# Kernel tuning notes

Measured on AMD Instinct MI355X. Metric: run time of the kernel, lower is better.

Reference implementation:

```python
import jax, jax.numpy as jnp
import numpy as np

D_MODEL = 2048
N_HEADS = 16
HEAD_DIM = D_MODEL // N_HEADS
SCALE = HEAD_DIM ** -0.5
LN_EPS = 1e-5
N_LAYERS = 24


def _layernorm(x, g, b):
    mu = jnp.mean(x, axis=-1, keepdims=True)
    var = jnp.mean(jnp.square(x - mu), axis=-1, keepdims=True)
    return (x - mu) * jax.lax.rsqrt(var + LN_EPS) * g + b


def _split_heads(x):  # [B,S,D] -> [B,H,S,hd]
    B, S, _ = x.shape
    return x.reshape(B, S, N_HEADS, HEAD_DIM).transpose(0, 2, 1, 3)


def setup_inputs() -> dict:
    key = jax.random.key(0)
    ks = jax.random.split(key, 12)
    B, St, Si = 2, 2048, 1024
    std_qkv = D_MODEL ** -0.5
    std_o = (2 * N_LAYERS) ** -0.5
    return {
        "q_text": jax.random.normal(ks[0], (B, St, D_MODEL), jnp.float32),
        "q_image": jax.random.normal(ks[1], (B, Si, D_MODEL), jnp.float32),
        "k_text": jax.random.normal(ks[2], (B, St, D_MODEL), jnp.float32),
        "k_image": jax.random.normal(ks[3], (B, Si, D_MODEL), jnp.float32),
        "Wq": jax.random.normal(ks[4], (D_MODEL, D_MODEL), jnp.float32) * std_qkv,
        "Wk": jax.random.normal(ks[5], (D_MODEL, D_MODEL), jnp.float32) * std_qkv,
        "Wv": jax.random.normal(ks[6], (D_MODEL, D_MODEL), jnp.float32) * std_qkv,
        "Wo": jax.random.normal(ks[7], (D_MODEL, D_MODEL), jnp.float32) * std_o,
        "ln_text_g": jnp.ones((D_MODEL,), jnp.float32),
        "ln_text_b": jnp.zeros((D_MODEL,), jnp.float32),
        "ln_image_g": jnp.ones((D_MODEL,), jnp.float32),
        "ln_image_b": jnp.zeros((D_MODEL,), jnp.float32),
    }


def reference(q_text, q_image, k_text, k_image, Wq, Wk, Wv, Wo,
              ln_text_g, ln_text_b, ln_image_g, ln_image_b):
    # Normalize each key modality once, project to K/V, concat along seq.
    kt = _layernorm(k_text, ln_text_g, ln_text_b)
    ki = _layernorm(k_image, ln_image_g, ln_image_b)
    concat_k = jnp.concatenate([_split_heads(kt @ Wk.T), _split_heads(ki @ Wk.T)], axis=2)
    concat_v = jnp.concatenate([_split_heads(kt @ Wv.T), _split_heads(ki @ Wv.T)], axis=2)

    def attend(q, g, b):
        B, S, _ = q.shape
        qn = _layernorm(q, g, b)
        qh = _split_heads(qn @ Wq.T) * SCALE            # [B,H,Sq,hd]
        scores = jnp.einsum('bhqd,bhkd->bhqk', qh, concat_k)
        attn = jax.nn.softmax(scores.astype(jnp.float32), axis=-1).astype(q.dtype)
        out = jnp.einsum('bhqk,bhkd->bhqd', attn, concat_v)
        out = out.transpose(0, 2, 1, 3).reshape(B, S, D_MODEL)
        return out @ Wo.T

    out_text = attend(q_text, ln_text_g, ln_text_b)
    out_image = attend(q_image, ln_image_g, ln_image_b)
    return (out_text, out_image)
```

## Files before the change

kernel.cpp:

```cpp
#include <hip/hip_runtime.h>

typedef __attribute__((ext_vector_type(8))) short bf16x8;
typedef __attribute__((ext_vector_type(4))) float f32x4;
typedef __attribute__((ext_vector_type(8))) unsigned short u16x8;
typedef __attribute__((ext_vector_type(4))) unsigned short u16x4;

#define D_MODEL 2048
#define NH 16
#define HD 128
#define SKV 3072
#define QK_SCALE 0.08838834764831845f

__device__ __forceinline__ unsigned short f2bf(float f) {
  unsigned int u = __float_as_uint(f);
  u += 0x7fffu + ((u >> 16) & 1u);
  return (unsigned short)(u >> 16);
}

typedef __attribute__((address_space(1))) void as1_void;
typedef __attribute__((address_space(3))) void as3_void;
__device__ __forceinline__ void gload_lds16(const void* g, void* l) {
  __builtin_amdgcn_global_load_lds((as1_void*)g, (as3_void*)l, 16, 0, 0);
}

#define MFMA16(a, b, c) __builtin_amdgcn_mfma_f32_16x16x32_bf16((a), (b), (c), 0, 0, 0)

__global__ __launch_bounds__(256) void cvt_w_kernel(
    const float* __restrict__ s0, const float* __restrict__ s1,
    const float* __restrict__ s2, const float* __restrict__ s3,
    unsigned short* __restrict__ dstbase) {
  const int y = blockIdx.y;
  const float* src = (y == 0) ? s0 : (y == 1) ? s1 : (y == 2) ? s2 : s3;
  const float scale = (y == 0) ? QK_SCALE : 1.0f;
  unsigned short* dst = dstbase + (size_t)y * 4194304;
  int i = blockIdx.x * 256 + threadIdx.x;
  const float4* s = (const float4*)src + (size_t)i * 2;
  float4 a = s[0], b = s[1];
  u16x8 r;
  r[0] = f2bf(a.x * scale); r[1] = f2bf(a.y * scale);
  r[2] = f2bf(a.z * scale); r[3] = f2bf(a.w * scale);
  r[4] = f2bf(b.x * scale); r[5] = f2bf(b.y * scale);
  r[6] = f2bf(b.z * scale); r[7] = f2bf(b.w * scale);
  *((u16x8*)dst + i) = r;
}

__global__ __launch_bounds__(256) void ln_kernel(
    const float* __restrict__ x, const float* __restrict__ gw,
    const float* __restrict__ bw, unsigned short* __restrict__ out,
    int spb, int orpb, int obase) {
  const int row = blockIdx.x;
  const int t = threadIdx.x;
  const int b = row / spb, s = row - b * spb;
  const float* xr = x + (size_t)row * D_MODEL;
  unsigned short* orow = out + ((size_t)b * orpb + obase + s) * D_MODEL;

  float4 v0 = *(const float4*)(xr + t * 8);
  float4 v1 = *(const float4*)(xr + t * 8 + 4);
  float sum = v0.x + v0.y + v0.z + v0.w + v1.x + v1.y + v1.z + v1.w;
  float sq  = v0.x*v0.x + v0.y*v0.y + v0.z*v0.z + v0.w*v0.w
            + v1.x*v1.x + v1.y*v1.y + v1.z*v1.z + v1.w*v1.w;
#pragma unroll
  for (int o = 32; o > 0; o >>= 1) {
    sum += __shfl_down(sum, o);
    sq  += __shfl_down(sq, o);
  }
  __shared__ float red[8];
  const int wv = t >> 6, l = t & 63;
  if (l == 0) { red[wv] = sum; red[4 + wv] = sq; }
  __syncthreads();
  sum = red[0] + red[1] + red[2] + red[3];
  sq  = red[4] + red[5] + red[6] + red[7];
  const float mu = sum * (1.0f / 2048.0f);
  const float var = sq * (1.0f / 2048.0f) - mu * mu;
  const float rs = rsqrtf(var + 1e-5f);

  float4 g0 = *(const float4*)(gw + t * 8);
  float4 g1 = *(const float4*)(gw + t * 8 + 4);
  float4 b0 = *(const float4*)(bw + t * 8);
  float4 b1 = *(const float4*)(bw + t * 8 + 4);
  u16x8 r;
  r[0] = f2bf((v0.x - mu) * rs * g0.x + b0.x);
  r[1] = f2bf((v0.y - mu) * rs * g0.y + b0.y);
  r[2] = f2bf((v0.z - mu) * rs * g0.z + b0.z);
  r[3] = f2bf((v0.w - mu) * rs * g0.w + b0.w);
  r[4] = f2bf((v1.x - mu) * rs * g1.x + b1.x);
  r[5] = f2bf((v1.y - mu) * rs * g1.y + b1.y);
  r[6] = f2bf((v1.z - mu) * rs * g1.z + b1.z);
  r[7] = f2bf((v1.w - mu) * rs * g1.w + b1.w);
  *(u16x8*)(orow + t * 8) = r;
}

__global__ __launch_bounds__(512, 2) void gemm256_kernel(
    const unsigned short* __restrict__ A,
    const unsigned short* __restrict__ W0, const unsigned short* __restrict__ W1,
    void* __restrict__ dst0, void* __restrict__ dst1, int mode) {
  __shared__ unsigned short lds[3][2][8192];

  const int tid = threadIdx.x;
  const int wid = tid >> 6, l = tid & 63;
  const int wm = wid >> 2, wn = wid & 3;
  const int fr = l & 15, fg = l >> 4;

  const int nwg = gridDim.x, cpx = nwg >> 3;
  const int bid = blockIdx.x;
  const int wg = (bid & 7) * cpx + (bid >> 3);
  const int bm = wg >> 3, bn = wg & 7;

  const unsigned short* Wp = W0;
  int m = mode;
  if (mode == 4) { if (blockIdx.y == 0) m = 3; else { m = 1; Wp = W1; } }

  const int srow = tid >> 2, scol = (tid & 3) * 8;
  const unsigned short* ga = A  + (size_t)(bm * 256 + srow) * 2048 + scol;
  const unsigned short* gb = Wp + (size_t)(bn * 256 + srow) * 2048 + scol;

#define STAGE(buf, kt) do {                                         \
    const int _ko = (kt) * 32;                                      \
    unsigned short* _la = &lds[(buf)][0][wid * 512];                \
    unsigned short* _lb = &lds[(buf)][1][wid * 512];                \
    gload_lds16(ga + _ko,              _la);                        \
    gload_lds16(ga + _ko + 128 * 2048, _la + 4096);                 \
    gload_lds16(gb + _ko,              _lb);                        \
    gload_lds16(gb + _ko + 128 * 2048, _lb + 4096);                 \
  } while (0)

  f32x4 acc[8][4] = {};

  STAGE(0, 0);
  STAGE(1, 1);
  asm volatile("s_waitcnt vmcnt(4)" ::: "memory");
  __builtin_amdgcn_s_barrier();

  int cur = 0;
  for (int kt = 0; kt < 64; ++kt) {
    bf16x8 af[8], bfr[4];
#pragma unroll
    for (int mi = 0; mi < 8; ++mi)
      af[mi] = *(const bf16x8*)&lds[cur][0][(wm * 128 + mi * 16 + fr) * 32 + fg * 8];
#pragma unroll
    for (int ni = 0; ni < 4; ++ni)
      bfr[ni] = *(const bf16x8*)&lds[cur][1][(wn * 64 + ni * 16 + fr) * 32 + fg * 8];

    if (kt < 62) {
      int sb = cur + 2; if (sb >= 3) sb -= 3;
      STAGE(sb, kt + 2);
    }

    __builtin_amdgcn_s_setprio(1);
#pragma unroll
    for (int mi = 0; mi < 8; ++mi)
#pragma unroll
      for (int ni = 0; ni < 4; ++ni)
        acc[mi][ni] = MFMA16(af[mi], bfr[ni], acc[mi][ni]);
    __builtin_amdgcn_s_setprio(0);

    __builtin_amdgcn_sched_barrier(0);
    if (kt < 62) {
      asm volatile("s_waitcnt vmcnt(4)" ::: "memory");
      __builtin_amdgcn_s_barrier();
    } else if (kt < 63) {
      asm volatile("s_waitcnt vmcnt(0)" ::: "memory");
      __builtin_amdgcn_s_barrier();
    }
    ++cur; if (cur >= 3) cur = 0;
  }
#undef STAGE

#pragma unroll
  for (int mi = 0; mi < 8; ++mi) {
#pragma unroll
    for (int r = 0; r < 4; ++r) {
      int row = bm * 256 + wm * 128 + mi * 16 + fg * 4 + r;
#pragma unroll
      for (int ni = 0; ni < 4; ++ni) {
        int col = bn * 256 + wn * 64 + ni * 16 + fr;
        float v = acc[mi][ni][r];
        if (m == 2) {
          ((float*)dst0)[(size_t)row * 2048 + col] = v;
        } else if (m == 0) {
          int hh = col >> 7, d = col & 127;
          if (row < 4096) {
            int b = row >> 11, s = row & 2047;
            ((unsigned short*)dst0)[((size_t)(b * NH + hh) * 2048 + s) * 128 + d] = f2bf(v);
          } else {
            int rr = row - 4096, b = rr >> 10, s = rr & 1023;
            ((unsigned short*)dst1)[((size_t)(b * NH + hh) * 1024 + s) * 128 + d] = f2bf(v);
          }
        } else {
          int b = row / 3072, s = row - b * 3072;
          int hh = col >> 7, d = col & 127;
          size_t bh = (size_t)(b * NH + hh);
          if (m == 3) {
            ((unsigned short*)dst0)[(bh * 3072 + s) * 128 + (d ^ ((s & 7) << 3))] = f2bf(v);
          } else {
            int ssw = (s & ~63) | ((s & 63) ^ ((d & 7) << 3));
            ((unsigned short*)dst1)[(bh * 128 + d) * (size_t)3072 + ssw] = f2bf(v);
          }
        }
      }
    }
  }
}

__global__ __launch_bounds__(256, 3) void attn_kernel(
    const unsigned short* __restrict__ Qt, const unsigned short* __restrict__ Qi,
    const unsigned short* __restrict__ Kh, const unsigned short* __restrict__ Vt,
    unsigned short* __restrict__ AOt, unsigned short* __restrict__ AOi) {
  __shared__ unsigned short Sh[24576];
  unsigned short* Ks = Sh;
  unsigned short* Vs = Sh + 8192;

  const int lin = blockIdx.x;
  const int w768 = (lin & 7) * 96 + (lin >> 3);
  const int qt24 = w768 % 24;
  const int hb   = w768 / 24;
  const int h = hb & 15, b = hb >> 4;
  const bool is_text = qt24 < 16;
  const int qt = is_text ? qt24 : qt24 - 16;
  const int Sq = is_text ? 2048 : 1024;
  const unsigned short* Qh = is_text ? Qt : Qi;
  unsigned short* AO = is_text ? AOt : AOi;

  const int tid = threadIdx.x;
  const int w = tid >> 6, l = tid & 63;
  const int fr = l & 15, fg = l >> 4;
  const size_t bh = (size_t)(b * NH + h);
  unsigned short* Pw = Sh + 16384 + w * 2048;

  const unsigned short* Qbase = Qh + (bh * Sq + (size_t)qt * 128 + w * 32) * HD;
  bf16x8 qf[2][4];
#pragma unroll
  for (int h2 = 0; h2 < 2; ++h2)
#pragma unroll
    for (int c = 0; c < 4; ++c)
      qf[h2][c] = *(const bf16x8*)(Qbase + (h2 * 16 + fr) * HD + c * 32 + fg * 8);

  f32x4 o[2][8] = {};
  float m[2]    = {-1e30f, -1e30f};
  float lsum[2] = {0.f, 0.f};

  const unsigned short* Kb = Kh + bh * (size_t)SKV * HD;
  const unsigned short* Vb = Vt + bh * (size_t)HD * SKV;

  const int krow = l >> 4, kcol = (l & 15) * 8;
  const int vrow = l >> 3, vcol = (l & 7) * 8;
  const int sw = (fr & 7) << 3;

  for (int kt = 0; kt < SKV / 64; ++kt) {
#pragma unroll
    for (int i = 0; i < 4; ++i) {
      const int ci = w * 4 + i;
      gload_lds16(Kb + (size_t)(kt * 64 + ci * 4 + krow) * HD + kcol, &Ks[ci * 512]);
      gload_lds16(Vb + (size_t)(ci * 8 + vrow) * SKV + kt * 64 + vcol, &Vs[ci * 512]);
    }
    __syncthreads();

    f32x4 sT[2][4] = {};
#pragma unroll
    for (int j = 0; j < 4; ++j) {
      const int krb = (j * 16 + fr) * 128;
#pragma unroll
      for (int c = 0; c < 4; ++c) {
        bf16x8 kf = *(const bf16x8*)&Ks[krb + ((c * 32 + fg * 8) ^ sw)];
        sT[0][j] = MFMA16(kf, qf[0][c], sT[0][j]);
        sT[1][j] = MFMA16(kf, qf[1][c], sT[1][j]);
      }
    }

#pragma unroll
    for (int h2 = 0; h2 < 2; ++h2) {
      float tm = sT[h2][0][0];
#pragma unroll
      for (int j = 0; j < 4; ++j)
#pragma unroll
        for (int r = 0; r < 4; ++r) tm = fmaxf(tm, sT[h2][j][r]);
      tm = fmaxf(tm, __shfl_xor(tm, 16));
      tm = fmaxf(tm, __shfl_xor(tm, 32));
      if (__any(tm - m[h2] > 8.0f)) {
        float mn = fmaxf(m[h2], tm);
        float al = __expf(m[h2] - mn);
#pragma unroll
        for (int nt = 0; nt < 8; ++nt) {
          f32x4 t = o[h2][nt];
          t[0] *= al; t[1] *= al; t[2] *= al; t[3] *= al;
          o[h2][nt] = t;
        }
        lsum[h2] *= al;
        m[h2] = mn;
      }
      const float mm = m[h2];
      float ps = 0.f;
      unsigned short* prow = &Pw[(h2 * 16 + fr) * 64];
#pragma unroll
      for (int j = 0; j < 4; ++j) {
        u16x4 pk;
#pragma unroll
        for (int r = 0; r < 4; ++r) {
          float p = __expf(sT[h2][j][r] - mm);
          ps += p;
          pk[r] = f2bf(p);
        }
        *reinterpret_cast<u16x4*>(&prow[(16 * j + fg * 4) ^ sw]) = pk;
      }
      lsum[h2] += ps;
    }

    asm volatile("s_waitcnt lgkmcnt(0)" ::: "memory");
    __builtin_amdgcn_sched_barrier(0);

    bf16x8 pb[2][2];
#pragma unroll
    for (int h2 = 0; h2 < 2; ++h2)
#pragma unroll
      for (int kc = 0; kc < 2; ++kc)
        pb[h2][kc] = *(const bf16x8*)&Pw[(h2 * 16 + fr) * 64 + ((kc * 32 + fg * 8) ^ sw)];
#pragma unroll
    for (int nt = 0; nt < 8; ++nt) {
      const int vrb = (nt * 16 + fr) * 64;
#pragma unroll
      for (int kc = 0; kc < 2; ++kc) {
        bf16x8 vf = *(const bf16x8*)&Vs[vrb + ((kc * 32 + fg * 8) ^ sw)];
        o[0][nt] = MFMA16(vf, pb[0][kc], o[0][nt]);
        o[1][nt] = MFMA16(vf, pb[1][kc], o[1][nt]);
      }
    }
    __syncthreads();
  }

  float inv[2];
#pragma unroll
  for (int h2 = 0; h2 < 2; ++h2) {
    float t = lsum[h2];
    t += __shfl_xor(t, 16);
    t += __shfl_xor(t, 32);
    inv[h2] = 1.0f / t;
  }
  unsigned short* Os = &Sh[w * 4096];
#pragma unroll
  for (int h2 = 0; h2 < 2; ++h2) {
    unsigned short* orow = &Os[(h2 * 16 + fr) * 128];
#pragma unroll
    for (int nt = 0; nt < 8; ++nt) {
      u16x4 pk;
#pragma unroll
      for (int r = 0; r < 4; ++r) pk[r] = f2bf(o[h2][nt][r] * inv[h2]);
      *reinterpret_cast<u16x4*>(&orow[(nt * 16 + fg * 4) ^ sw]) = pk;
    }
  }
  asm volatile("s_waitcnt lgkmcnt(0)" ::: "memory");
  __builtin_amdgcn_sched_barrier(0);
  const int qr4 = l >> 4;
  const int dc = (l & 15) * 8;
  unsigned short* AObase = AO + ((size_t)b * Sq + (size_t)qt * 128 + w * 32) * D_MODEL + h * HD;
#pragma unroll
  for (int g = 0; g < 8; ++g) {
    const int row = g * 4 + qr4;
    bf16x8 v = *reinterpret_cast<const bf16x8*>(&Os[row * 128 + (dc ^ ((row & 7) << 3))]);
    *reinterpret_cast<bf16x8*>(&AObase[(size_t)row * D_MODEL + dc]) = v;
  }
}

extern "C" void kernel_launch(void* const* d_in, const int* in_sizes, int n_in,
                              void* d_out, int out_size, void* d_ws, size_t ws_size,
                              hipStream_t stream) {
  const float* q_text  = (const float*)d_in[0];
  const float* q_image = (const float*)d_in[1];
  const float* k_text  = (const float*)d_in[2];
  const float* k_image = (const float*)d_in[3];
  const float* Wq = (const float*)d_in[4];
  const float* Wk = (const float*)d_in[5];
  const float* Wv = (const float*)d_in[6];
  const float* Wo = (const float*)d_in[7];
  const float* ln_tg = (const float*)d_in[8];
  const float* ln_tb = (const float*)d_in[9];
  const float* ln_ig = (const float*)d_in[10];
  const float* ln_ib = (const float*)d_in[11];

  unsigned short* wq  = (unsigned short*)d_ws;
  unsigned short* wk  = wq  + 4194304;
  unsigned short* wv  = wk  + 4194304;
  unsigned short* wo  = wv  + 4194304;
  unsigned short* xqt = wo  + 4194304;
  unsigned short* xqi = xqt + 8388608;
  unsigned short* xk  = xqi + 4194304;
  unsigned short* qht = xk  + 12582912;
  unsigned short* qhi = qht + 8388608;
  unsigned short* kh  = qhi + 4194304;
  unsigned short* vt  = kh  + 12582912;
  const size_t needed = (size_t)(vt + 12582912 - wq) * 2;
  if (ws_size < needed) return;

  cvt_w_kernel<<<dim3(2048, 4), 256, 0, stream>>>(Wq, Wk, Wv, Wo, wq);

  ln_kernel<<<4096, 256, 0, stream>>>(q_text,  ln_tg, ln_tb, xqt, 2048, 2048, 0);
  ln_kernel<<<2048, 256, 0, stream>>>(q_image, ln_ig, ln_ib, xqi, 1024, 1024, 0);
  ln_kernel<<<4096, 256, 0, stream>>>(k_text,  ln_tg, ln_tb, xk, 2048, 3072, 0);
  ln_kernel<<<2048, 256, 0, stream>>>(k_image, ln_ig, ln_ib, xk, 1024, 3072, 2048);

  gemm256_kernel<<<192, 512, 0, stream>>>(xqt, wq, nullptr, qht, qhi, 0);
  gemm256_kernel<<<dim3(192, 2), 512, 0, stream>>>(xk, wk, wv, kh, vt, 4);

  attn_kernel<<<768, 256, 0, stream>>>(qht, qhi, kh, vt, xqt, xqi);

  gemm256_kernel<<<192, 512, 0, stream>>>(xqt, wo, nullptr, d_out, nullptr, 2);
}
```

Baseline: 538.6 us.

## Shrink GEMM tiles, merge Q/K/V projections, and pipeline attention with exp2

The GEMM moves from 256x256 tiles with 512 threads to 128x128 tiles with 256 threads, and the Q, K and V projections are merged into one launch of 2304 blocks. This is meant to improve occupancy and wave balance across CUs. The attention kernel now uses 32-wide KV tiles with double-buffered K/V staging and explicit barriers. It also folds log2(e) into the Q weights so it can use hardware v_exp_f32, packs to bf16 with v_cvt_pk, and raises the threshold for deferring the max rescale. Smaller tiles raise global traffic per FLOP, and the shorter KV step doubles the number of barriers per iteration.

```diff
diff --git a/kernel.cpp b/kernel.cpp
--- a/kernel.cpp
+++ b/kernel.cpp
@@ -3,18 +3,25 @@
 typedef __attribute__((ext_vector_type(8))) short bf16x8;
 typedef __attribute__((ext_vector_type(4))) float f32x4;
 typedef __attribute__((ext_vector_type(8))) unsigned short u16x8;
-typedef __attribute__((ext_vector_type(4))) unsigned short u16x4;
 
 #define D_MODEL 2048
 #define NH 16
 #define HD 128
 #define SKV 3072
 #define QK_SCALE 0.08838834764831845f
+#define LOG2E 1.4426950408889634f
+#define DEFER_THR 11.5413f
 
 __device__ __forceinline__ unsigned short f2bf(float f) {
   unsigned int u = __float_as_uint(f);
   u += 0x7fffu + ((u >> 16) & 1u);
   return (unsigned short)(u >> 16);
+}
+__device__ __forceinline__ float exp2hw(float x) {
+  float r; asm("v_exp_f32 %0, %1" : "=v"(r) : "v"(x)); return r;
+}
+__device__ __forceinline__ unsigned int cvtpk(float lo, float hi) {
+  unsigned int r; asm("v_cvt_pk_bf16_f32 %0, %1, %2" : "=v"(r) : "v"(lo), "v"(hi)); return r;
 }
 
 typedef __attribute__((address_space(1))) void as1_void;
@@ -31,7 +38,7 @@
     unsigned short* __restrict__ dstbase) {
   const int y = blockIdx.y;
   const float* src = (y == 0) ? s0 : (y == 1) ? s1 : (y == 2) ? s2 : s3;
-  const float scale = (y == 0) ? QK_SCALE : 1.0f;
+  const float scale = (y == 0) ? (QK_SCALE * LOG2E) : 1.0f;
   unsigned short* dst = dstbase + (size_t)y * 4194304;
   int i = blockIdx.x * 256 + threadIdx.x;
   const float4* s = (const float4*)src + (size_t)i * 2;
@@ -90,41 +97,47 @@
   *(u16x8*)(orow + t * 8) = r;
 }
 
-__global__ __launch_bounds__(512, 2) void gemm256_kernel(
-    const unsigned short* __restrict__ A,
-    const unsigned short* __restrict__ W0, const unsigned short* __restrict__ W1,
-    void* __restrict__ dst0, void* __restrict__ dst1, int mode) {
-  __shared__ unsigned short lds[3][2][8192];
+__global__ __launch_bounds__(256, 3) void gemm128_kernel(
+    const unsigned short* __restrict__ Aq, const unsigned short* __restrict__ Akv,
+    const unsigned short* __restrict__ Wq, const unsigned short* __restrict__ Wk,
+    const unsigned short* __restrict__ Wv,
+    void* __restrict__ d0, void* __restrict__ d1,
+    void* __restrict__ d2, void* __restrict__ d3, int mode) {
+  __shared__ unsigned short lds[3][2][4096];
 
   const int tid = threadIdx.x;
   const int wid = tid >> 6, l = tid & 63;
-  const int wm = wid >> 2, wn = wid & 3;
+  const int wm = wid >> 1, wn = wid & 1;
   const int fr = l & 15, fg = l >> 4;
 
-  const int nwg = gridDim.x, cpx = nwg >> 3;
-  const int bid = blockIdx.x;
-  const int wg = (bid & 7) * cpx + (bid >> 3);
-  const int bm = wg >> 3, bn = wg & 7;
-
-  const unsigned short* Wp = W0;
-  int m = mode;
-  if (mode == 4) { if (blockIdx.y == 0) m = 3; else { m = 1; Wp = W1; } }
-
-  const int srow = tid >> 2, scol = (tid & 3) * 8;
-  const unsigned short* ga = A  + (size_t)(bm * 256 + srow) * 2048 + scol;
-  const unsigned short* gb = Wp + (size_t)(bn * 256 + srow) * 2048 + scol;
-
-#define STAGE(buf, kt) do {                                         \
-    const int _ko = (kt) * 32;                                      \
-    unsigned short* _la = &lds[(buf)][0][wid * 512];                \
-    unsigned short* _lb = &lds[(buf)][1][wid * 512];                \
-    gload_lds16(ga + _ko,              _la);                        \
-    gload_lds16(ga + _ko + 128 * 2048, _la + 4096);                 \
-    gload_lds16(gb + _ko,              _lb);                        \
-    gload_lds16(gb + _ko + 128 * 2048, _lb + 4096);                 \
+  const int cpx = gridDim.x >> 3;
+  int wg = (blockIdx.x & 7) * cpx + (blockIdx.x >> 3);
+
+  const unsigned short* A = Aq;
+  const unsigned short* W = Wq;
+  int emode = mode;
+  if (mode == 10) {
+    int mat = wg / 768; wg -= mat * 768;
+    if (mat == 0)      { emode = 0; }
+    else if (mat == 1) { emode = 3; A = Akv; W = Wk; }
+    else               { emode = 1; A = Akv; W = Wv; }
+  }
+  const int bm = wg >> 4, bn = wg & 15;
+
+  const unsigned short* ga = A + (size_t)(bm * 128 + wid * 32 + (l >> 2)) * 2048 + (l & 3) * 8;
+  const unsigned short* gb = W + (size_t)(bn * 128 + wid * 32 + (l >> 2)) * 2048 + (l & 3) * 8;
+
+#define STAGE(buf, kt) do {                                   \
+    const int _ko = (kt) * 32;                                \
+    unsigned short* _la = &lds[(buf)][0][wid * 1024];         \
+    unsigned short* _lb = &lds[(buf)][1][wid * 1024];         \
+    gload_lds16(ga + _ko,             _la);                   \
+    gload_lds16(ga + _ko + 16 * 2048, _la + 512);             \
+    gload_lds16(gb + _ko,             _lb);                   \
+    gload_lds16(gb + _ko + 16 * 2048, _lb + 512);             \
   } while (0)
 
-  f32x4 acc[8][4] = {};
+  f32x4 acc[4][4] = {};
 
   STAGE(0, 0);
   STAGE(1, 1);
@@ -133,10 +146,10 @@
 
   int cur = 0;
   for (int kt = 0; kt < 64; ++kt) {
-    bf16x8 af[8], bfr[4];
-#pragma unroll
-    for (int mi = 0; mi < 8; ++mi)
-      af[mi] = *(const bf16x8*)&lds[cur][0][(wm * 128 + mi * 16 + fr) * 32 + fg * 8];
+    bf16x8 af[4], bfr[4];
+#pragma unroll
+    for (int mi = 0; mi < 4; ++mi)
+      af[mi] = *(const bf16x8*)&lds[cur][0][(wm * 64 + mi * 16 + fr) * 32 + fg * 8];
 #pragma unroll
     for (int ni = 0; ni < 4; ++ni)
       bfr[ni] = *(const bf16x8*)&lds[cur][1][(wn * 64 + ni * 16 + fr) * 32 + fg * 8];
@@ -148,7 +161,7 @@
 
     __builtin_amdgcn_s_setprio(1);
 #pragma unroll
-    for (int mi = 0; mi < 8; ++mi)
+    for (int mi = 0; mi < 4; ++mi)
 #pragma unroll
       for (int ni = 0; ni < 4; ++ni)
         acc[mi][ni] = MFMA16(af[mi], bfr[ni], acc[mi][ni]);
@@ -167,34 +180,34 @@
 #undef STAGE
 
 #pragma unroll
-  for (int mi = 0; mi < 8; ++mi) {
+  for (int mi = 0; mi < 4; ++mi) {
 #pragma unroll
     for (int r = 0; r < 4; ++r) {
-      int row = bm * 256 + wm * 128 + mi * 16 + fg * 4 + r;
+      int row = bm * 128 + wm * 64 + mi * 16 + fg * 4 + r;
 #pragma unroll
       for (int ni = 0; ni < 4; ++ni) {
-        int col = bn * 256 + wn * 64 + ni * 16 + fr;
+        int col = bn * 128 + wn * 64 + ni * 16 + fr;
         float v = acc[mi][ni][r];
-        if (m == 2) {
-          ((float*)dst0)[(size_t)row * 2048 + col] = v;
-        } else if (m == 0) {
+        if (emode == 2) {
+          ((float*)d0)[(size_t)row * 2048 + col] = v;
+        } else if (emode == 0) {
           int hh = col >> 7, d = col & 127;
           if (row < 4096) {
             int b = row >> 11, s = row & 2047;
-            ((unsigned short*)dst0)[((size_t)(b * NH + hh) * 2048 + s) * 128 + d] = f2bf(v);
+            ((unsigned short*)d0)[((size_t)(b * NH + hh) * 2048 + s) * 128 + d] = f2bf(v);
           } else {
             int rr = row - 4096, b = rr >> 10, s = rr & 1023;
-            ((unsigned short*)dst1)[((size_t)(b * NH + hh) * 1024 + s) * 128 + d] = f2bf(v);
+            ((unsigned short*)d1)[((size_t)(b * NH + hh) * 1024 + s) * 128 + d] = f2bf(v);
           }
         } else {
           int b = row / 3072, s = row - b * 3072;
           int hh = col >> 7, d = col & 127;
           size_t bh = (size_t)(b * NH + hh);
-          if (m == 3) {
-            ((unsigned short*)dst0)[(bh * 3072 + s) * 128 + (d ^ ((s & 7) << 3))] = f2bf(v);
+          if (emode == 3) {
+            ((unsigned short*)d2)[(bh * 3072 + s) * 128 + (d ^ ((s & 7) << 3))] = f2bf(v);
           } else {
-            int ssw = (s & ~63) | ((s & 63) ^ ((d & 7) << 3));
-            ((unsigned short*)dst1)[(bh * 128 + d) * (size_t)3072 + ssw] = f2bf(v);
+            int ssw = (s & ~31) | ((s & 31) ^ ((d & 3) << 3));
+            ((unsigned short*)d3)[(bh * 128 + d) * (size_t)3072 + ssw] = f2bf(v);
           }
         }
       }
@@ -206,9 +219,7 @@
     const unsigned short* __restrict__ Qt, const unsigned short* __restrict__ Qi,
     const unsigned short* __restrict__ Kh, const unsigned short* __restrict__ Vt,
     unsigned short* __restrict__ AOt, unsigned short* __restrict__ AOi) {
-  __shared__ unsigned short Sh[24576];
-  unsigned short* Ks = Sh;
-  unsigned short* Vs = Sh + 8192;
+  __shared__ unsigned short Sh[20480];
 
   const int lin = blockIdx.x;
   const int w768 = (lin & 7) * 96 + (lin >> 3);
@@ -225,7 +236,7 @@
   const int w = tid >> 6, l = tid & 63;
   const int fr = l & 15, fg = l >> 4;
   const size_t bh = (size_t)(b * NH + h);
-  unsigned short* Pw = Sh + 16384 + w * 2048;
+  unsigned short* Pw = Sh + 16384 + w * 1024;
 
   const unsigned short* Qbase = Qh + (bh * Sq + (size_t)qt * 128 + w * 32) * HD;
   bf16x8 qf[2][4];
@@ -242,43 +253,56 @@
   const unsigned short* Kb = Kh + bh * (size_t)SKV * HD;
   const unsigned short* Vb = Vt + bh * (size_t)HD * SKV;
 
-  const int krow = l >> 4, kcol = (l & 15) * 8;
-  const int vrow = l >> 3, vcol = (l & 7) * 8;
-  const int sw = (fr & 7) << 3;
-
-  for (int kt = 0; kt < SKV / 64; ++kt) {
-#pragma unroll
-    for (int i = 0; i < 4; ++i) {
-      const int ci = w * 4 + i;
-      gload_lds16(Kb + (size_t)(kt * 64 + ci * 4 + krow) * HD + kcol, &Ks[ci * 512]);
-      gload_lds16(Vb + (size_t)(ci * 8 + vrow) * SKV + kt * 64 + vcol, &Vs[ci * 512]);
-    }
-    __syncthreads();
-
-    f32x4 sT[2][4] = {};
-#pragma unroll
-    for (int j = 0; j < 4; ++j) {
+  const int swk = (fr & 7) << 3;
+  const int swv = (fr & 3) << 3;
+
+#define STAGE_K(kt, half) do {                                                   \
+    unsigned short* _d = Sh + (half) * 4096 + w * 1024;                          \
+    const unsigned short* _s = Kb + (size_t)((kt) * 32 + w * 8 + (l >> 4)) * 128 \
+                               + (l & 15) * 8;                                   \
+    gload_lds16(_s, _d);                                                         \
+    gload_lds16(_s + 4 * 128, _d + 512);                                         \
+  } while (0)
+#define STAGE_V(kt, half) do {                                                   \
+    unsigned short* _d = Sh + 8192 + (half) * 4096 + w * 1024;                   \
+    const unsigned short* _s = Vb + (size_t)(w * 32 + (l >> 2)) * SKV            \
+                               + (kt) * 32 + (l & 3) * 8;                        \
+    gload_lds16(_s, _d);                                                         \
+    gload_lds16(_s + 16 * SKV, _d + 512);                                        \
+  } while (0)
+
+  STAGE_K(0, 0);
+  for (int kt = 0; kt < 96; ++kt) {
+    const int half = kt & 1;
+    STAGE_V(kt, half);
+    asm volatile("s_waitcnt vmcnt(2)" ::: "memory");
+    __builtin_amdgcn_s_barrier();
+
+    const unsigned short* Ksc = Sh + half * 4096;
+    f32x4 sT[2][2] = {};
+#pragma unroll
+    for (int j = 0; j < 2; ++j) {
       const int krb = (j * 16 + fr) * 128;
 #pragma unroll
       for (int c = 0; c < 4; ++c) {
-        bf16x8 kf = *(const bf16x8*)&Ks[krb + ((c * 32 + fg * 8) ^ sw)];
+        bf16x8 kf = *(const bf16x8*)&Ksc[krb + ((c * 32 + fg * 8) ^ swk)];
         sT[0][j] = MFMA16(kf, qf[0][c], sT[0][j]);
         sT[1][j] = MFMA16(kf, qf[1][c], sT[1][j]);
       }
     }
+    if (kt < 95) STAGE_K(kt + 1, half ^ 1);
 
 #pragma unroll
     for (int h2 = 0; h2 < 2; ++h2) {
-      float tm = sT[h2][0][0];
-#pragma unroll
-      for (int j = 0; j < 4; ++j)
-#pragma unroll
-        for (int r = 0; r < 4; ++r) tm = fmaxf(tm, sT[h2][j][r]);
+      float tm = fmaxf(fmaxf(fmaxf(sT[h2][0][0], sT[h2][0][1]),
+                             fmaxf(sT[h2][0][2], sT[h2][0][3])),
+                       fmaxf(fmaxf(sT[h2][1][0], sT[h2][1][1]),
+                             fmaxf(sT[h2][1][2], sT[h2][1][3])));
       tm = fmaxf(tm, __shfl_xor(tm, 16));
       tm = fmaxf(tm, __shfl_xor(tm, 32));
-      if (__any(tm - m[h2] > 8.0f)) {
+      if (__any(tm - m[h2] > DEFER_THR)) {
         float mn = fmaxf(m[h2], tm);
-        float al = __expf(m[h2] - mn);
+        float al = exp2hw(m[h2] - mn);
 #pragma unroll
         for (int nt = 0; nt < 8; ++nt) {
           f32x4 t = o[h2][nt];
@@ -289,43 +313,40 @@
         m[h2] = mn;
       }
       const float mm = m[h2];
-      float ps = 0.f;
-      unsigned short* prow = &Pw[(h2 * 16 + fr) * 64];
-#pragma unroll
-      for (int j = 0; j < 4; ++j) {
-        u16x4 pk;
-#pragma unroll
-        for (int r = 0; r < 4; ++r) {
-          float p = __expf(sT[h2][j][r] - mm);
-          ps += p;
-          pk[r] = f2bf(p);
-        }
-        *reinterpret_cast<u16x4*>(&prow[(16 * j + fg * 4) ^ sw]) = pk;
-      }
-      lsum[h2] += ps;
-    }
+      float p00 = exp2hw(sT[h2][0][0] - mm), p01 = exp2hw(sT[h2][0][1] - mm);
+      float p02 = exp2hw(sT[h2][0][2] - mm), p03 = exp2hw(sT[h2][0][3] - mm);
+      float p10 = exp2hw(sT[h2][1][0] - mm), p11 = exp2hw(sT[h2][1][1] - mm);
+      float p12 = exp2hw(sT[h2][1][2] - mm), p13 = exp2hw(sT[h2][1][3] - mm);
+      lsum[h2] += (p00 + p01 + p02 + p03) + (p10 + p11 + p12 + p13);
+      unsigned short* prow = &Pw[(h2 * 16 + fr) * 32];
+      uint2 w0; w0.x = cvtpk(p00, p01); w0.y = cvtpk(p02, p03);
+      uint2 w1; w1.x = cvtpk(p10, p11); w1.y = cvtpk(p12, p13);
+      *(uint2*)(prow + ((fg * 4) ^ swv))      = w0;
+      *(uint2*)(prow + ((16 + fg * 4) ^ swv)) = w1;
+    }
+
+    if (kt < 95) asm volatile("s_waitcnt vmcnt(2)" ::: "memory");
+    else         asm volatile("s_waitcnt vmcnt(0)" ::: "memory");
+    __builtin_amdgcn_s_barrier();
 
     asm volatile("s_waitcnt lgkmcnt(0)" ::: "memory");
     __builtin_amdgcn_sched_barrier(0);
 
-    bf16x8 pb[2][2];
+    const unsigned short* Vsc = Sh + 8192 + half * 4096;
+    bf16x8 pb[2];
 #pragma unroll
     for (int h2 = 0; h2 < 2; ++h2)
-#pragma unroll
-      for (int kc = 0; kc < 2; ++kc)
-        pb[h2][kc] = *(const bf16x8*)&Pw[(h2 * 16 + fr) * 64 + ((kc * 32 + fg * 8) ^ sw)];
+      pb[h2] = *(const bf16x8*)&Pw[(h2 * 16 + fr) * 32 + ((fg * 8) ^ swv)];
 #pragma unroll
     for (int nt = 0; nt < 8; ++nt) {
-      const int vrb = (nt * 16 + fr) * 64;
-#pragma unroll
-      for (int kc = 0; kc < 2; ++kc) {
-        bf16x8 vf = *(const bf16x8*)&Vs[vrb + ((kc * 32 + fg * 8) ^ sw)];
-        o[0][nt] = MFMA16(vf, pb[0][kc], o[0][nt]);
-        o[1][nt] = MFMA16(vf, pb[1][kc], o[1][nt]);
-      }
-    }
-    __syncthreads();
-  }
+      bf16x8 vf = *(const bf16x8*)&Vsc[(nt * 16 + fr) * 32 + ((fg * 8) ^ swv)];
+      o[0][nt] = MFMA16(vf, pb[0], o[0][nt]);
+      o[1][nt] = MFMA16(vf, pb[1], o[1][nt]);
+    }
+    __builtin_amdgcn_s_barrier();
+  }
+#undef STAGE_K
+#undef STAGE_V
 
   float inv[2];
 #pragma unroll
@@ -339,12 +360,13 @@
 #pragma unroll
   for (int h2 = 0; h2 < 2; ++h2) {
     unsigned short* orow = &Os[(h2 * 16 + fr) * 128];
+    const int sw8 = (fr & 7) << 3;
 #pragma unroll
     for (int nt = 0; nt < 8; ++nt) {
-      u16x4 pk;
-#pragma unroll
-      for (int r = 0; r < 4; ++r) pk[r] = f2bf(o[h2][nt][r] * inv[h2]);
-      *reinterpret_cast<u16x4*>(&orow[(nt * 16 + fg * 4) ^ sw]) = pk;
+      uint2 pk;
+      pk.x = cvtpk(o[h2][nt][0] * inv[h2], o[h2][nt][1] * inv[h2]);
+      pk.y = cvtpk(o[h2][nt][2] * inv[h2], o[h2][nt][3] * inv[h2]);
+      *(uint2*)(orow + ((nt * 16 + fg * 4) ^ sw8)) = pk;
     }
   }
   asm volatile("s_waitcnt lgkmcnt(0)" ::: "memory");
@@ -397,10 +419,10 @@
   ln_kernel<<<4096, 256, 0, stream>>>(k_text,  ln_tg, ln_tb, xk, 2048, 3072, 0);
   ln_kernel<<<2048, 256, 0, stream>>>(k_image, ln_ig, ln_ib, xk, 1024, 3072, 2048);
 
-  gemm256_kernel<<<192, 512, 0, stream>>>(xqt, wq, nullptr, qht, qhi, 0);
-  gemm256_kernel<<<dim3(192, 2), 512, 0, stream>>>(xk, wk, wv, kh, vt, 4);
+  gemm128_kernel<<<2304, 256, 0, stream>>>(xqt, xk, wq, wk, wv, qht, qhi, kh, vt, 10);
 
   attn_kernel<<<768, 256, 0, stream>>>(qht, qhi, kh, vt, xqt, xqi);
 
-  gemm256_kernel<<<192, 512, 0, stream>>>(xqt, wo, nullptr, d_out, nullptr, 2);
-}
+  gemm128_kernel<<<768, 256, 0, stream>>>(xqt, nullptr, wo, nullptr, nullptr,
+                                          d_out, nullptr, nullptr, nullptr, 2);
+}
```

After: 531.8 us. No clear change (-1.2%).
